# Performance work log

Hardware: AMD Instinct MI355X
Metric: run time of the kernel (lower is better)

Reference implementation:

```python
import jax, jax.numpy as jnp
import numpy as np

N_NODES = 20000
N_EDGES = 320000
HEAD_NUM = 4
IN_DIM = 64  # per-head dim


def setup_inputs() -> dict:
    key = jax.random.key(0)
    k1, k2, k3, k4 = jax.random.split(key, 4)
    h = jax.random.normal(k1, (N_NODES, HEAD_NUM * IN_DIM), dtype=jnp.float32)
    W_gate = jax.random.normal(k2, (1, 2 * IN_DIM), dtype=jnp.float32) * (1.414 / np.sqrt(2 * IN_DIM))
    b_gate = jnp.zeros((1,), dtype=jnp.float32)
    src = jax.random.randint(k3, (N_EDGES,), 0, N_NODES, dtype=jnp.int64)
    dst = jax.random.randint(k4, (N_EDGES,), 0, N_NODES, dtype=jnp.int64)
    return {"h": h, "W_gate": W_gate, "b_gate": b_gate, "src": src, "dst": dst}


def reference(h, W_gate, b_gate, src, dst):
    N = h.shape[0]
    E = src.shape[0]
    # in-degree norm: deg = in_degrees (count of dst occurrences), clamp >= 1, d = deg^-0.5
    deg = jax.ops.segment_sum(jnp.ones((E,), dtype=h.dtype), dst, num_segments=N)
    norm = jnp.clip(deg, 1.0, None) ** -0.5  # [N]

    hr = h.reshape(N, HEAD_NUM, IN_DIM)
    h1 = hr[dst]  # dst features [E, H, D]
    h2 = hr[src]  # src features [E, H, D]
    # gate(cat(h1, h2)) with W_gate [1, 2D]: split into dst/src halves
    Wd = W_gate[0, :IN_DIM]
    Ws = W_gate[0, IN_DIM:]
    s = jnp.tanh(jnp.einsum('ehd,d->eh', h1, Wd) + jnp.einsum('ehd,d->eh', h2, Ws) + b_gate[0])  # [E, H]
    s = s * norm[dst][:, None] * norm[src][:, None]
    e_h = h2 * s[..., None]  # [E, H, D]
    # scatter-sum edge messages to destination nodes (copy_e + sum)
    z = jax.ops.segment_sum(e_h.reshape(E, HEAD_NUM * IN_DIM), dst, num_segments=N)
    return z
```

## Files before the change

kernel.cpp:

```cpp
#include <hip/hip_runtime.h>
#include <hip/hip_bf16.h>

#define N_NODES 20000
#define N_EDGES 320000
#define HEADS   4
#define FEAT    256
#define BCAP    64

typedef unsigned short u16x8 __attribute__((ext_vector_type(8)));
typedef float f32x4 __attribute__((ext_vector_type(4)));

__device__ __forceinline__ float fast_tanh(float x) {
    float e = __expf(2.0f * x);
    float r = __builtin_amdgcn_rcpf(e + 1.0f);
    return 1.0f - 2.0f * r;
}

__global__ void zero_deg_kernel(int* __restrict__ deg) {
    int i = blockIdx.x * blockDim.x + threadIdx.x;
    if (i < N_NODES) deg[i] = 0;
}

__global__ void prep_kernel(const float* __restrict__ h,
                            const float* __restrict__ Wg,
                            const int* __restrict__ src,
                            const int* __restrict__ dst,
                            float* __restrict__ gd,
                            float* __restrict__ gs,
                            unsigned short* __restrict__ hb,
                            int* __restrict__ deg,
                            unsigned short* __restrict__ bucket) {
    int t = threadIdx.x;
    int node = blockIdx.x * 4 + (t >> 6);
    int lane = t & 63;
    int head = lane >> 4;
    int d16 = lane & 15;

    const float4* h4 = (const float4*)h;
    const float4* Wg4 = (const float4*)Wg;
    float4 v = h4[(size_t)node * 64 + lane];
    float4 wd = Wg4[d16];
    float4 ws = Wg4[16 + d16];

    ushort4 o;
    o.x = __bfloat16_as_ushort(__float2bfloat16(v.x));
    o.y = __bfloat16_as_ushort(__float2bfloat16(v.y));
    o.z = __bfloat16_as_ushort(__float2bfloat16(v.z));
    o.w = __bfloat16_as_ushort(__float2bfloat16(v.w));
    ((ushort4*)hb)[(size_t)node * 64 + lane] = o;

    if (t < 64) {
        int eid = blockIdx.x * 64 + t;
        int dn = dst[eid];
        int r = atomicAdd(&deg[dn], 1);
        if (r < BCAP) bucket[dn * BCAP + r] = (unsigned short)src[eid];
    }

    float a = v.x * wd.x + v.y * wd.y + v.z * wd.z + v.w * wd.w;
    float b = v.x * ws.x + v.y * ws.y + v.z * ws.z + v.w * ws.w;
#pragma unroll
    for (int off = 1; off < 16; off <<= 1) {
        a += __shfl_xor(a, off);
        b += __shfl_xor(b, off);
    }
    if (d16 == 0) {
        gd[node * HEADS + head] = a;
        gs[node * HEADS + head] = b;
    }
}

__global__ void gather_kernel(const unsigned short* __restrict__ hb,
                              const int* __restrict__ deg,
                              const unsigned short* __restrict__ bucket,
                              const float* __restrict__ gd,
                              const float* __restrict__ gs,
                              const float* __restrict__ bg,
                              float* __restrict__ z) {
    int wid = (blockIdx.x * blockDim.x + threadIdx.x) >> 6;
    int lane = threadIdx.x & 63;
    if (wid >= N_NODES) return;
    int half = lane >> 5;
    int l32 = lane & 31;
    int head = l32 >> 3;

    int dv = deg[wid];
    int degc = min(dv, BCAP);
    float nd = rsqrtf(fmaxf((float)dv, 1.0f));
    float gb = gd[wid * HEADS + head] + bg[0];

    int sv = (int)bucket[wid * BCAP + lane];

    const u16x8* h8 = (const u16x8*)hb;

    float acc[8];
#pragma unroll
    for (int j = 0; j < 8; ++j) acc[j] = 0.f;

    int iters = (degc + 1) >> 1;
#pragma unroll 4
    for (int k = 0; k < iters; ++k) {
        int e = 2 * k + half;
        bool valid = (e < degc);
        int sn = __shfl(sv, e);
        if (!valid) sn = 0;
        float gsv = gs[sn * HEADS + head];
        float ns = rsqrtf(fmaxf((float)deg[sn], 1.0f));
        u16x8 r = h8[(size_t)sn * 32 + l32];
        float g = valid ? fast_tanh(gb + gsv) * nd * ns : 0.f;
#pragma unroll
        for (int j = 0; j < 8; ++j)
            acc[j] += g * __uint_as_float((unsigned)r[j] << 16);
    }
#pragma unroll
    for (int j = 0; j < 8; ++j) acc[j] += __shfl_xor(acc[j], 32);

    f32x4 out;
    int jb = half * 4;
    out.x = acc[jb]; out.y = acc[jb + 1]; out.z = acc[jb + 2]; out.w = acc[jb + 3];
    ((f32x4*)z)[(size_t)wid * 64 + l32 * 2 + half] = out;
}

extern "C" void kernel_launch(void* const* d_in, const int* in_sizes, int n_in,
                              void* d_out, int out_size, void* d_ws, size_t ws_size,
                              hipStream_t stream) {
    const float* h      = (const float*)d_in[0];
    const float* W_gate = (const float*)d_in[1];
    const float* b_gate = (const float*)d_in[2];
    const int*   src    = (const int*)d_in[3];
    const int*   dst    = (const int*)d_in[4];
    float* z = (float*)d_out;

    char* p = (char*)d_ws;
    int*   deg    = (int*)p;              p += 80000;
    float* gd     = (float*)p;            p += 320000;
    float* gs     = (float*)p;            p += 320000;
    unsigned short* bucket = (unsigned short*)p; p += 2560000;
    unsigned short* hb = (unsigned short*)p; p += 10240000;

    zero_deg_kernel<<<(N_NODES + 255) / 256, 256, 0, stream>>>(deg);
    prep_kernel<<<N_NODES / 4, 256, 0, stream>>>(h, W_gate, src, dst, gd, gs, hb, deg, bucket);
    gather_kernel<<<(N_NODES * 64 + 255) / 256, 256, 0, stream>>>(
        hb, deg, bucket, gd, gs, b_gate, z);
}
```

Baseline: 57.97 us.

## Fuse zero, prep and gather stages into one cooperative persistent kernel

Merges the three kernel launches into one cooperative kernel with 1024 persistent blocks, separated by two grid-wide syncs. Each stage becomes a grid-stride loop over nodes or blocks. This removes launch overhead and inter-kernel gaps. In exchange it adds grid-barrier cost and limits the gather phase to a fixed number of resident waves, which can reduce latency hiding for the irregular gathers.

Result: slower. 224.9 us (+288.0%).

```diff
diff --git a/kernel.cpp b/kernel.cpp
--- a/kernel.cpp
+++ b/kernel.cpp
@@ -1,11 +1,17 @@
 #include <hip/hip_runtime.h>
 #include <hip/hip_bf16.h>
+#include <hip/hip_cooperative_groups.h>
+
+namespace cg = cooperative_groups;
 
 #define N_NODES 20000
 #define N_EDGES 320000
 #define HEADS   4
-#define FEAT    256
 #define BCAP    64
+#define NBLK    1024
+#define TPB     256
+#define NWAVES  (NBLK * TPB / 64)
+#define PREP_VBLKS 5000
 
 typedef unsigned short u16x8 __attribute__((ext_vector_type(8)));
 typedef float f32x4 __attribute__((ext_vector_type(4)));
@@ -16,108 +22,112 @@
     return 1.0f - 2.0f * r;
 }
 
-__global__ void zero_deg_kernel(int* __restrict__ deg) {
-    int i = blockIdx.x * blockDim.x + threadIdx.x;
-    if (i < N_NODES) deg[i] = 0;
-}
+__global__ __launch_bounds__(TPB, 4) void fused_kernel(
+    const float* __restrict__ h,
+    const float* __restrict__ Wg,
+    const float* __restrict__ bg,
+    const int* __restrict__ src,
+    const int* __restrict__ dst,
+    float* __restrict__ gd,
+    float* __restrict__ gs,
+    unsigned short* __restrict__ hb,
+    int* __restrict__ deg,
+    unsigned short* __restrict__ bucket,
+    float* __restrict__ z)
+{
+    cg::grid_group grid = cg::this_grid();
+    int t = threadIdx.x;
+    int lane = t & 63;
+    int gthread = blockIdx.x * TPB + t;
 
-__global__ void prep_kernel(const float* __restrict__ h,
-                            const float* __restrict__ Wg,
-                            const int* __restrict__ src,
-                            const int* __restrict__ dst,
-                            float* __restrict__ gd,
-                            float* __restrict__ gs,
-                            unsigned short* __restrict__ hb,
-                            int* __restrict__ deg,
-                            unsigned short* __restrict__ bucket) {
-    int t = threadIdx.x;
-    int node = blockIdx.x * 4 + (t >> 6);
-    int lane = t & 63;
-    int head = lane >> 4;
-    int d16 = lane & 15;
+    for (int i = gthread; i < N_NODES; i += NBLK * TPB) deg[i] = 0;
+    grid.sync();
 
-    const float4* h4 = (const float4*)h;
-    const float4* Wg4 = (const float4*)Wg;
-    float4 v = h4[(size_t)node * 64 + lane];
-    float4 wd = Wg4[d16];
-    float4 ws = Wg4[16 + d16];
+    {
+        int head = lane >> 4;
+        int d16 = lane & 15;
+        const float4* h4 = (const float4*)h;
+        const float4* Wg4 = (const float4*)Wg;
+        float4 wd = Wg4[d16];
+        float4 ws = Wg4[16 + d16];
 
-    ushort4 o;
-    o.x = __bfloat16_as_ushort(__float2bfloat16(v.x));
-    o.y = __bfloat16_as_ushort(__float2bfloat16(v.y));
-    o.z = __bfloat16_as_ushort(__float2bfloat16(v.z));
-    o.w = __bfloat16_as_ushort(__float2bfloat16(v.w));
-    ((ushort4*)hb)[(size_t)node * 64 + lane] = o;
+        for (int v = blockIdx.x; v < PREP_VBLKS; v += NBLK) {
+            int node = v * 4 + (t >> 6);
+            float4 hv = h4[(size_t)node * 64 + lane];
 
-    if (t < 64) {
-        int eid = blockIdx.x * 64 + t;
-        int dn = dst[eid];
-        int r = atomicAdd(&deg[dn], 1);
-        if (r < BCAP) bucket[dn * BCAP + r] = (unsigned short)src[eid];
+            ushort4 o;
+            o.x = __bfloat16_as_ushort(__float2bfloat16(hv.x));
+            o.y = __bfloat16_as_ushort(__float2bfloat16(hv.y));
+            o.z = __bfloat16_as_ushort(__float2bfloat16(hv.z));
+            o.w = __bfloat16_as_ushort(__float2bfloat16(hv.w));
+            ((ushort4*)hb)[(size_t)node * 64 + lane] = o;
+
+            if (t < 64) {
+                int eid = v * 64 + t;
+                int dn = dst[eid];
+                int r = atomicAdd(&deg[dn], 1);
+                if (r < BCAP) bucket[dn * BCAP + r] = (unsigned short)src[eid];
+            }
+
+            float a = hv.x * wd.x + hv.y * wd.y + hv.z * wd.z + hv.w * wd.w;
+            float b = hv.x * ws.x + hv.y * ws.y + hv.z * ws.z + hv.w * ws.w;
+#pragma unroll
+            for (int off = 1; off < 16; off <<= 1) {
+                a += __shfl_xor(a, off);
+                b += __shfl_xor(b, off);
+            }
+            if (d16 == 0) {
+                gd[node * HEADS + head] = a;
+                gs[node * HEADS + head] = b;
+            }
+        }
     }
+    grid.sync();
 
-    float a = v.x * wd.x + v.y * wd.y + v.z * wd.z + v.w * wd.w;
-    float b = v.x * ws.x + v.y * ws.y + v.z * ws.z + v.w * ws.w;
+    {
+        int half = lane >> 5;
+        int l32 = lane & 31;
+        int head = l32 >> 3;
+        float bias = bg[0];
+        const u16x8* h8 = (const u16x8*)hb;
+        int w0 = gthread >> 6;
+
+        for (int w = w0; w < N_NODES; w += NWAVES) {
+            int dv = deg[w];
+            int degc = min(dv, BCAP);
+            float nd = rsqrtf(fmaxf((float)dv, 1.0f));
+            float gb = gd[w * HEADS + head] + bias;
+
+            int sv = (int)bucket[w * BCAP + lane];
+
+            float acc[8];
 #pragma unroll
-    for (int off = 1; off < 16; off <<= 1) {
-        a += __shfl_xor(a, off);
-        b += __shfl_xor(b, off);
+            for (int j = 0; j < 8; ++j) acc[j] = 0.f;
+
+            int iters = (degc + 1) >> 1;
+#pragma unroll 4
+            for (int k = 0; k < iters; ++k) {
+                int e = 2 * k + half;
+                bool valid = (e < degc);
+                int sn = __shfl(sv, e);
+                if (!valid) sn = 0;
+                float gsv = gs[sn * HEADS + head];
+                float ns = rsqrtf(fmaxf((float)deg[sn], 1.0f));
+                u16x8 r = h8[(size_t)sn * 32 + l32];
+                float g = valid ? fast_tanh(gb + gsv) * nd * ns : 0.f;
+#pragma unroll
+                for (int j = 0; j < 8; ++j)
+                    acc[j] += g * __uint_as_float((unsigned)r[j] << 16);
+            }
+#pragma unroll
+            for (int j = 0; j < 8; ++j) acc[j] += __shfl_xor(acc[j], 32);
+
+            f32x4 out;
+            int jb = half * 4;
+            out.x = acc[jb]; out.y = acc[jb + 1]; out.z = acc[jb + 2]; out.w = acc[jb + 3];
+            ((f32x4*)z)[(size_t)w * 64 + l32 * 2 + half] = out;
+        }
     }
-    if (d16 == 0) {
-        gd[node * HEADS + head] = a;
-        gs[node * HEADS + head] = b;
-    }
-}
-
-__global__ void gather_kernel(const unsigned short* __restrict__ hb,
-                              const int* __restrict__ deg,
-                              const unsigned short* __restrict__ bucket,
-                              const float* __restrict__ gd,
-                              const float* __restrict__ gs,
-                              const float* __restrict__ bg,
-                              float* __restrict__ z) {
-    int wid = (blockIdx.x * blockDim.x + threadIdx.x) >> 6;
-    int lane = threadIdx.x & 63;
-    if (wid >= N_NODES) return;
-    int half = lane >> 5;
-    int l32 = lane & 31;
-    int head = l32 >> 3;
-
-    int dv = deg[wid];
-    int degc = min(dv, BCAP);
-    float nd = rsqrtf(fmaxf((float)dv, 1.0f));
-    float gb = gd[wid * HEADS + head] + bg[0];
-
-    int sv = (int)bucket[wid * BCAP + lane];
-
-    const u16x8* h8 = (const u16x8*)hb;
-
-    float acc[8];
-#pragma unroll
-    for (int j = 0; j < 8; ++j) acc[j] = 0.f;
-
-    int iters = (degc + 1) >> 1;
-#pragma unroll 4
-    for (int k = 0; k < iters; ++k) {
-        int e = 2 * k + half;
-        bool valid = (e < degc);
-        int sn = __shfl(sv, e);
-        if (!valid) sn = 0;
-        float gsv = gs[sn * HEADS + head];
-        float ns = rsqrtf(fmaxf((float)deg[sn], 1.0f));
-        u16x8 r = h8[(size_t)sn * 32 + l32];
-        float g = valid ? fast_tanh(gb + gsv) * nd * ns : 0.f;
-#pragma unroll
-        for (int j = 0; j < 8; ++j)
-            acc[j] += g * __uint_as_float((unsigned)r[j] << 16);
-    }
-#pragma unroll
-    for (int j = 0; j < 8; ++j) acc[j] += __shfl_xor(acc[j], 32);
-
-    f32x4 out;
-    int jb = half * 4;
-    out.x = acc[jb]; out.y = acc[jb + 1]; out.z = acc[jb + 2]; out.w = acc[jb + 3];
-    ((f32x4*)z)[(size_t)wid * 64 + l32 * 2 + half] = out;
 }
 
 extern "C" void kernel_launch(void* const* d_in, const int* in_sizes, int n_in,
@@ -137,8 +147,10 @@
     unsigned short* bucket = (unsigned short*)p; p += 2560000;
     unsigned short* hb = (unsigned short*)p; p += 10240000;
 
-    zero_deg_kernel<<<(N_NODES + 255) / 256, 256, 0, stream>>>(deg);
-    prep_kernel<<<N_NODES / 4, 256, 0, stream>>>(h, W_gate, src, dst, gd, gs, hb, deg, bucket);
-    gather_kernel<<<(N_NODES * 64 + 255) / 256, 256, 0, stream>>>(
-        hb, deg, bucket, gd, gs, b_gate, z);
+    void* args[] = {
+        (void*)&h, (void*)&W_gate, (void*)&b_gate, (void*)&src, (void*)&dst,
+        (void*)&gd, (void*)&gs, (void*)&hb, (void*)&deg, (void*)&bucket, (void*)&z
+    };
+    hipLaunchCooperativeKernel((void*)fused_kernel, dim3(NBLK), dim3(TPB),
+                               args, 0, stream);
 }
```

## Store bf16 features head-major and gather one head per block slice

Applied to the files above, without the earlier changes.

The bf16 copy of node features is stored head-major ([head][node][64]), so each head's table is a contiguous 2.5 MB slab. The gather kernel now launches four times as many waves. Each wave handles one node and one head, with 8 groups of 8 lanes pulling 128-byte rows from 8 edges at once. Block ordering interleaves heads so concurrently running blocks touch a single head's slab, which is meant to improve L2 locality. In exchange, the per-edge gate and degree loads are repeated for each head, a three-step cross-group shuffle reduction is added, and only 8 lanes perform the output stores.

Result: slower. 64.06 us (+10.5%).

```diff
diff --git a/kernel.cpp b/kernel.cpp
--- a/kernel.cpp
+++ b/kernel.cpp
@@ -4,7 +4,6 @@
 #define N_NODES 20000
 #define N_EDGES 320000
 #define HEADS   4
-#define FEAT    256
 #define BCAP    64
 
 typedef unsigned short u16x8 __attribute__((ext_vector_type(8)));
@@ -47,7 +46,7 @@
     o.y = __bfloat16_as_ushort(__float2bfloat16(v.y));
     o.z = __bfloat16_as_ushort(__float2bfloat16(v.z));
     o.w = __bfloat16_as_ushort(__float2bfloat16(v.w));
-    ((ushort4*)hb)[(size_t)node * 64 + lane] = o;
+    ((ushort4*)hb)[((size_t)head * N_NODES + node) * 16 + d16] = o;
 
     if (t < 64) {
         int eid = blockIdx.x * 64 + t;
@@ -76,48 +75,56 @@
                               const float* __restrict__ gs,
                               const float* __restrict__ bg,
                               float* __restrict__ z) {
-    int wid = (blockIdx.x * blockDim.x + threadIdx.x) >> 6;
-    int lane = threadIdx.x & 63;
-    if (wid >= N_NODES) return;
-    int half = lane >> 5;
-    int l32 = lane & 31;
-    int head = l32 >> 3;
+    int b = blockIdx.x;
+    int t = threadIdx.x;
+    int lane = t & 63;
+    int g8 = b >> 3;
+    int r  = b & 7;
+    int hd = r >> 1;
+    int node = (g8 * 2 + (r & 1)) * 4 + (t >> 6);
+    int group = lane >> 3;
+    int gl = lane & 7;
 
-    int dv = deg[wid];
+    int dv = deg[node];
     int degc = min(dv, BCAP);
     float nd = rsqrtf(fmaxf((float)dv, 1.0f));
-    float gb = gd[wid * HEADS + head] + bg[0];
+    float gb = gd[node * HEADS + hd] + bg[0];
 
-    int sv = (int)bucket[wid * BCAP + lane];
+    int sv = (int)bucket[node * BCAP + lane];
 
-    const u16x8* h8 = (const u16x8*)hb;
+    const u16x8* h8 = (const u16x8*)hb + (size_t)hd * N_NODES * 8;
 
     float acc[8];
 #pragma unroll
     for (int j = 0; j < 8; ++j) acc[j] = 0.f;
 
-    int iters = (degc + 1) >> 1;
-#pragma unroll 4
+    int iters = (degc + 7) >> 3;
+#pragma unroll 2
     for (int k = 0; k < iters; ++k) {
-        int e = 2 * k + half;
+        int e = k * 8 + group;
         bool valid = (e < degc);
         int sn = __shfl(sv, e);
         if (!valid) sn = 0;
-        float gsv = gs[sn * HEADS + head];
+        float gsv = gs[sn * HEADS + hd];
         float ns = rsqrtf(fmaxf((float)deg[sn], 1.0f));
-        u16x8 r = h8[(size_t)sn * 32 + l32];
+        u16x8 rr = h8[(size_t)sn * 8 + gl];
         float g = valid ? fast_tanh(gb + gsv) * nd * ns : 0.f;
 #pragma unroll
         for (int j = 0; j < 8; ++j)
-            acc[j] += g * __uint_as_float((unsigned)r[j] << 16);
+            acc[j] += g * __uint_as_float((unsigned)rr[j] << 16);
     }
 #pragma unroll
-    for (int j = 0; j < 8; ++j) acc[j] += __shfl_xor(acc[j], 32);
+    for (int off = 8; off < 64; off <<= 1)
+#pragma unroll
+        for (int j = 0; j < 8; ++j) acc[j] += __shfl_xor(acc[j], off);
 
-    f32x4 out;
-    int jb = half * 4;
-    out.x = acc[jb]; out.y = acc[jb + 1]; out.z = acc[jb + 2]; out.w = acc[jb + 3];
-    ((f32x4*)z)[(size_t)wid * 64 + l32 * 2 + half] = out;
+    if (lane < 8) {
+        size_t base = ((size_t)node * 256 + hd * 64 + lane * 8) >> 2;
+        f32x4 o0 = {acc[0], acc[1], acc[2], acc[3]};
+        f32x4 o1 = {acc[4], acc[5], acc[6], acc[7]};
+        ((f32x4*)z)[base] = o0;
+        ((f32x4*)z)[base + 1] = o1;
+    }
 }
 
 extern "C" void kernel_launch(void* const* d_in, const int* in_sizes, int n_in,
@@ -139,6 +146,5 @@
 
     zero_deg_kernel<<<(N_NODES + 255) / 256, 256, 0, stream>>>(deg);
     prep_kernel<<<N_NODES / 4, 256, 0, stream>>>(h, W_gate, src, dst, gd, gs, hb, deg, bucket);
-    gather_kernel<<<(N_NODES * 64 + 255) / 256, 256, 0, stream>>>(
-        hb, deg, bucket, gd, gs, b_gate, z);
+    gather_kernel<<<N_NODES, 256, 0, stream>>>(hb, deg, bucket, gd, gs, b_gate, z);
 }
```

## Process eight edges per wave with 32-feature lanes in gather kernel

Applied to the files above, without the earlier changes.

The gather kernel now assigns each group of 8 lanes to one edge, so 8 edges are in flight per iteration. Each lane loads four 16-byte chunks (32 bf16 features) instead of one, and there are fewer loop iterations. In exchange it needs a 3-step cross-lane shuffle reduction over 32 accumulators, uses more registers, and only 8 lanes issue the output stores. The edge bucketing atomics in prep are moved earlier so they are issued before the feature load.

After: 59.41 us. 1.02x slower.

```diff
diff --git a/kernel.cpp b/kernel.cpp
--- a/kernel.cpp
+++ b/kernel.cpp
@@ -4,7 +4,6 @@
 #define N_NODES 20000
 #define N_EDGES 320000
 #define HEADS   4
-#define FEAT    256
 #define BCAP    64
 
 typedef unsigned short u16x8 __attribute__((ext_vector_type(8)));
@@ -36,6 +35,14 @@
     int head = lane >> 4;
     int d16 = lane & 15;
 
+    if (t < 64) {
+        int eid = blockIdx.x * 64 + t;
+        int dn = dst[eid];
+        int sn = src[eid];
+        int r = atomicAdd(&deg[dn], 1);
+        if (r < BCAP) bucket[dn * BCAP + r] = (unsigned short)sn;
+    }
+
     const float4* h4 = (const float4*)h;
     const float4* Wg4 = (const float4*)Wg;
     float4 v = h4[(size_t)node * 64 + lane];
@@ -48,13 +55,6 @@
     o.z = __bfloat16_as_ushort(__float2bfloat16(v.z));
     o.w = __bfloat16_as_ushort(__float2bfloat16(v.w));
     ((ushort4*)hb)[(size_t)node * 64 + lane] = o;
-
-    if (t < 64) {
-        int eid = blockIdx.x * 64 + t;
-        int dn = dst[eid];
-        int r = atomicAdd(&deg[dn], 1);
-        if (r < BCAP) bucket[dn * BCAP + r] = (unsigned short)src[eid];
-    }
 
     float a = v.x * wd.x + v.y * wd.y + v.z * wd.z + v.w * wd.w;
     float b = v.x * ws.x + v.y * ws.y + v.z * ws.z + v.w * ws.w;
@@ -79,45 +79,64 @@
     int wid = (blockIdx.x * blockDim.x + threadIdx.x) >> 6;
     int lane = threadIdx.x & 63;
     if (wid >= N_NODES) return;
-    int half = lane >> 5;
-    int l32 = lane & 31;
-    int head = l32 >> 3;
+    int s  = lane >> 3;
+    int fl = lane & 7;
+    int head = fl >> 1;
+
+    int sv = (int)bucket[wid * BCAP + lane];
 
     int dv = deg[wid];
     int degc = min(dv, BCAP);
     float nd = rsqrtf(fmaxf((float)dv, 1.0f));
     float gb = gd[wid * HEADS + head] + bg[0];
 
-    int sv = (int)bucket[wid * BCAP + lane];
-
     const u16x8* h8 = (const u16x8*)hb;
 
-    float acc[8];
+    float acc[4][8];
 #pragma unroll
-    for (int j = 0; j < 8; ++j) acc[j] = 0.f;
+    for (int c = 0; c < 4; ++c)
+#pragma unroll
+        for (int j = 0; j < 8; ++j) acc[c][j] = 0.f;
 
-    int iters = (degc + 1) >> 1;
+    int iters = (degc + 7) >> 3;
 #pragma unroll 4
     for (int k = 0; k < iters; ++k) {
-        int e = 2 * k + half;
+        int e = 8 * k + s;
         bool valid = (e < degc);
         int sn = __shfl(sv, e);
         if (!valid) sn = 0;
         float gsv = gs[sn * HEADS + head];
         float ns = rsqrtf(fmaxf((float)deg[sn], 1.0f));
-        u16x8 r = h8[(size_t)sn * 32 + l32];
+        u16x8 r0 = h8[(size_t)sn * 32 + fl * 4];
+        u16x8 r1 = h8[(size_t)sn * 32 + fl * 4 + 1];
+        u16x8 r2 = h8[(size_t)sn * 32 + fl * 4 + 2];
+        u16x8 r3 = h8[(size_t)sn * 32 + fl * 4 + 3];
         float g = valid ? fast_tanh(gb + gsv) * nd * ns : 0.f;
 #pragma unroll
-        for (int j = 0; j < 8; ++j)
-            acc[j] += g * __uint_as_float((unsigned)r[j] << 16);
+        for (int j = 0; j < 8; ++j) {
+            acc[0][j] += g * __uint_as_float((unsigned)r0[j] << 16);
+            acc[1][j] += g * __uint_as_float((unsigned)r1[j] << 16);
+            acc[2][j] += g * __uint_as_float((unsigned)r2[j] << 16);
+            acc[3][j] += g * __uint_as_float((unsigned)r3[j] << 16);
+        }
     }
 #pragma unroll
-    for (int j = 0; j < 8; ++j) acc[j] += __shfl_xor(acc[j], 32);
+    for (int off = 8; off < 64; off <<= 1)
+#pragma unroll
+        for (int c = 0; c < 4; ++c)
+#pragma unroll
+            for (int j = 0; j < 8; ++j) acc[c][j] += __shfl_xor(acc[c][j], off);
 
-    f32x4 out;
-    int jb = half * 4;
-    out.x = acc[jb]; out.y = acc[jb + 1]; out.z = acc[jb + 2]; out.w = acc[jb + 3];
-    ((f32x4*)z)[(size_t)wid * 64 + l32 * 2 + half] = out;
+    if (lane < 8) {
+        size_t base = (size_t)wid * 64 + fl * 8;
+#pragma unroll
+        for (int c = 0; c < 4; ++c) {
+            f32x4 o0 = {acc[c][0], acc[c][1], acc[c][2], acc[c][3]};
+            f32x4 o1 = {acc[c][4], acc[c][5], acc[c][6], acc[c][7]};
+            ((f32x4*)z)[base + c * 2]     = o0;
+            ((f32x4*)z)[base + c * 2 + 1] = o1;
+        }
+    }
 }
 
 extern "C" void kernel_launch(void* const* d_in, const int* in_sizes, int n_in,
```
